# Performance work log

Hardware: AMD Instinct MI355X
Metric: run time of the kernel (lower is better)

The kernel has to match this reference:

```python
import jax, jax.numpy as jnp
import numpy as np

VOCAB = 4096   # vocab_size; must equal dim for weight + A@B to typecheck (as in source)
DIM = 4096
RANK = 256     # lora_rank
BATCH, SEQ = 4, 2048


def setup_inputs() -> dict:
    key = jax.random.key(0)
    k1, k2, k3, k4, k5 = jax.random.split(key, 5)
    x = jax.random.randint(k1, (BATCH, SEQ), 0, VOCAB)
    padding_mask = jax.random.randint(k2, (BATCH, SEQ), 0, 2).astype(bool)
    weight = jax.random.normal(k3, (VOCAB, DIM), dtype=jnp.float32) * 0.02
    A = jax.random.normal(k4, (VOCAB, RANK), dtype=jnp.float32) * 0.01
    B = jax.random.normal(k5, (RANK, VOCAB), dtype=jnp.float32) * 0.01
    return {"x": x, "padding_mask": padding_mask, "weight": weight, "A": A, "B": B}


def reference(x, padding_mask, weight, A, B):
    # world_size == 1, rank == 0 in the source module, so the distributed
    # index-shift / mask / all_reduce branches are no-ops.
    # lora_rank > 0 branch: embedding against the LoRA-corrected weight.
    # NOTE: faithful to source, A@B is [V, V] and requires DIM == VOCAB.
    corrected = weight + A @ B            # [V, DIM]
    y = corrected[x]                      # gather rows -> [B, S, DIM]
    # y[padding_mask] = 0
    y = jnp.where(padding_mask[..., None], jnp.zeros((), dtype=y.dtype), y)
    return y
```

## Files before the change

### kernel.cpp

```cpp
#include <hip/hip_runtime.h>
#include <stdint.h>

#define NTOK 8192
#define NCOL 4096
#define RANK 256
#define TPB  256
#define CPB  256

typedef __attribute__((ext_vector_type(8))) short bf16x8;
typedef __attribute__((ext_vector_type(4))) float f32x4;

__device__ __forceinline__ unsigned short f2bf(float f) {
    unsigned int u = __float_as_uint(f);
    u += 0x7fffu + ((u >> 16) & 1u);
    return (unsigned short)(u >> 16);
}

__global__ __launch_bounds__(256) void prep_kernel(
    const float* __restrict__ A, const float* __restrict__ B,
    unsigned short* __restrict__ Abf, unsigned short* __restrict__ Bfrag)
{
    if (blockIdx.x < 1024) {
        int i = blockIdx.x * 256 + threadIdx.x;
        float4 v = reinterpret_cast<const float4*>(A)[i];
        ushort4 o;
        o.x = f2bf(v.x); o.y = f2bf(v.y); o.z = f2bf(v.z); o.w = f2bf(v.w);
        reinterpret_cast<ushort4*>(Abf)[i] = o;
    } else {
        int gt = (blockIdx.x - 1024) * 256 + threadIdx.x;
        int ct = gt >> 9;
        int rem = gt & 511;
        int ks = rem >> 6;
        int ln = rem & 63;
        int col = ct * 16 + (ln & 15);
        int kb  = ks * 32 + ((ln >> 4) << 3);
        unsigned short pk[8];
        #pragma unroll
        for (int j = 0; j < 8; ++j)
            pk[j] = f2bf(B[(size_t)(kb + j) * NCOL + col]);
        uint4 o;
        o.x = (unsigned)pk[0] | ((unsigned)pk[1] << 16);
        o.y = (unsigned)pk[2] | ((unsigned)pk[3] << 16);
        o.z = (unsigned)pk[4] | ((unsigned)pk[5] << 16);
        o.w = (unsigned)pk[6] | ((unsigned)pk[7] << 16);
        reinterpret_cast<uint4*>(Bfrag)[gt] = o;
    }
}

__global__ __launch_bounds__(256) void emb_lora_mfma(
    const int* __restrict__ x,
    const int* __restrict__ mask,
    const float* __restrict__ W,
    const unsigned short* __restrict__ Abf,
    const unsigned short* __restrict__ Bfrag,
    float* __restrict__ out)
{
    __shared__ int s_idx[TPB];
    __shared__ int s_msk[TPB];

    const int tid  = threadIdx.x;
    const int lane = tid & 63;
    const int wave = tid >> 6;
    const int tok0 = blockIdx.x * TPB;
    const int col0 = blockIdx.y * CPB;

    s_idx[tid] = x[tok0 + tid];
    s_msk[tid] = mask[tok0 + tid];
    __syncthreads();

    bf16x8 af[4][8];
    #pragma unroll
    for (int g = 0; g < 4; ++g) {
        const int ar = s_idx[wave * 64 + g * 16 + (lane & 15)];
        const unsigned short* ap = Abf + (size_t)ar * RANK + ((lane >> 4) << 3);
        #pragma unroll
        for (int s = 0; s < 8; ++s)
            af[g][s] = *reinterpret_cast<const bf16x8*>(ap + s * 32);
    }

    const int colb = col0 + (lane & 15);
    unsigned mbits = 0;
    unsigned woff[4][4];
    unsigned obase[4];
    #pragma unroll
    for (int g = 0; g < 4; ++g) {
        const int rb = wave * 64 + g * 16 + ((lane >> 4) << 2);
        obase[g] = (unsigned)(tok0 + rb) * NCOL + colb;
        #pragma unroll
        for (int r = 0; r < 4; ++r) {
            mbits |= (s_msk[rb + r] ? 1u : 0u) << (g * 4 + r);
            woff[g][r] = (unsigned)s_idx[rb + r] * NCOL + colb;
        }
    }

    const uint4* bcol = reinterpret_cast<const uint4*>(Bfrag)
                        + (size_t)(blockIdx.y * 16) * 512 + lane;

    float wv[3][4][4];
    #pragma unroll
    for (int p = 0; p < 2; ++p) {
        #pragma unroll
        for (int g = 0; g < 4; ++g) {
            #pragma unroll
            for (int r = 0; r < 4; ++r) {
                float v = 0.0f;
                if (!((mbits >> (g * 4 + r)) & 1u)) v = W[woff[g][r] + p * 16];
                wv[p][g][r] = v;
            }
        }
    }

#define TILE_BODY(T, PF)                                                  \
    {                                                                     \
        const int t_ = (T);                                               \
        uint4 bb[4];                                                      \
        _Pragma("unroll")                                                 \
        for (int s = 0; s < 4; ++s)                                       \
            bb[s] = bcol[t_ * 512 + s * 64];                              \
        if (PF) {                                                         \
            _Pragma("unroll")                                             \
            for (int g = 0; g < 4; ++g) {                                 \
                _Pragma("unroll")                                         \
                for (int r = 0; r < 4; ++r) {                             \
                    float v = 0.0f;                                       \
                    if (!((mbits >> (g * 4 + r)) & 1u))                   \
                        v = W[woff[g][r] + (t_ + 2) * 16];                \
                    wv[(T + 2) % 3][g][r] = v;                            \
                }                                                         \
            }                                                             \
        }                                                                 \
        f32x4 acc[4];                                                     \
        _Pragma("unroll")                                                 \
        for (int g = 0; g < 4; ++g) acc[g] = (f32x4){0.f, 0.f, 0.f, 0.f}; \
        _Pragma("unroll")                                                 \
        for (int s = 0; s < 4; ++s) {                                     \
            bf16x8 b = __builtin_bit_cast(bf16x8, bb[s]);                 \
            _Pragma("unroll")                                             \
            for (int g = 0; g < 4; ++g)                                   \
                acc[g] = __builtin_amdgcn_mfma_f32_16x16x32_bf16(         \
                    af[g][s], b, acc[g], 0, 0, 0);                        \
        }                                                                 \
        _Pragma("unroll")                                                 \
        for (int s = 0; s < 4; ++s)                                       \
            bb[s] = bcol[t_ * 512 + (s + 4) * 64];                        \
        _Pragma("unroll")                                                 \
        for (int s = 0; s < 4; ++s) {                                     \
            bf16x8 b = __builtin_bit_cast(bf16x8, bb[s]);                 \
            _Pragma("unroll")                                             \
            for (int g = 0; g < 4; ++g)                                   \
                acc[g] = __builtin_amdgcn_mfma_f32_16x16x32_bf16(         \
                    af[g][s + 4], b, acc[g], 0, 0, 0);                    \
        }                                                                 \
        _Pragma("unroll")                                                 \
        for (int g = 0; g < 4; ++g) {                                     \
            _Pragma("unroll")                                             \
            for (int r = 0; r < 4; ++r) {                                 \
                float v = 0.0f;                                           \
                if (!((mbits >> (g * 4 + r)) & 1u))                       \
                    v = acc[g][r] + wv[(T) % 3][g][r];                    \
                out[obase[g] + r * NCOL + t_ * 16] = v;                   \
            }                                                             \
        }                                                                 \
    }

    TILE_BODY(0, 1);  TILE_BODY(1, 1);  TILE_BODY(2, 1);  TILE_BODY(3, 1);
    TILE_BODY(4, 1);  TILE_BODY(5, 1);  TILE_BODY(6, 1);  TILE_BODY(7, 1);
    TILE_BODY(8, 1);  TILE_BODY(9, 1);  TILE_BODY(10, 1); TILE_BODY(11, 1);
    TILE_BODY(12, 1); TILE_BODY(13, 1);
    TILE_BODY(14, 0); TILE_BODY(15, 0);
#undef TILE_BODY
}

extern "C" void kernel_launch(void* const* d_in, const int* in_sizes, int n_in,
                              void* d_out, int out_size, void* d_ws, size_t ws_size,
                              hipStream_t stream) {
    (void)in_sizes; (void)n_in; (void)out_size; (void)ws_size;

    const int*   x    = (const int*)d_in[0];
    const int*   mask = (const int*)d_in[1];
    const float* W    = (const float*)d_in[2];
    const float* A    = (const float*)d_in[3];
    const float* B    = (const float*)d_in[4];
    float*       out  = (float*)d_out;

    unsigned short* Abf   = (unsigned short*)d_ws;
    unsigned short* Bfrag = (unsigned short*)((char*)d_ws + (2u << 20));

    prep_kernel<<<dim3(1536), dim3(256), 0, stream>>>(A, B, Abf, Bfrag);

    dim3 grid(NTOK / TPB, NCOL / CPB);
    emb_lora_mfma<<<grid, dim3(256), 0, stream>>>(x, mask, W, Abf, Bfrag, out);
}
```

Before: 60.35 us.

## Transpose MFMA operands for float4 row-contiguous W loads and output stores

Swaps the A and B operands of the MFMA so each lane's accumulator holds four consecutive columns of one token row. W loads and output stores can then be 16-byte float4 accesses with one mask bit per row group instead of scalar strided ones. Columns per block are halved to 128, doubling the grid and re-gathering the A fragments twice as often, and the W prefetch ring shrinks from three stages to two.

New measurement: 72.62 us. 20.3% more time.

```diff
diff --git a/kernel.cpp b/kernel.cpp
--- a/kernel.cpp
+++ b/kernel.cpp
@@ -5,7 +5,7 @@
 #define NCOL 4096
 #define RANK 256
 #define TPB  256
-#define CPB  256
+#define CPB  128
 
 typedef __attribute__((ext_vector_type(8))) short bf16x8;
 typedef __attribute__((ext_vector_type(4))) float f32x4;
@@ -69,64 +69,59 @@
     __syncthreads();
 
     bf16x8 af[4][8];
+    int tokidx[4];
+    unsigned mb = 0;
     #pragma unroll
     for (int g = 0; g < 4; ++g) {
-        const int ar = s_idx[wave * 64 + g * 16 + (lane & 15)];
-        const unsigned short* ap = Abf + (size_t)ar * RANK + ((lane >> 4) << 3);
+        const int trow = wave * 64 + g * 16 + (lane & 15);
+        tokidx[g] = s_idx[trow];
+        mb |= (s_msk[trow] ? 1u : 0u) << g;
+        const unsigned short* ap = Abf + (size_t)tokidx[g] * RANK + ((lane >> 4) << 3);
         #pragma unroll
         for (int s = 0; s < 8; ++s)
             af[g][s] = *reinterpret_cast<const bf16x8*>(ap + s * 32);
     }
 
-    const int colb = col0 + (lane & 15);
-    unsigned mbits = 0;
-    unsigned woff[4][4];
-    unsigned obase[4];
+    const int colq = col0 + ((lane >> 4) << 2);
+    unsigned wq[4], oq[4];
     #pragma unroll
     for (int g = 0; g < 4; ++g) {
-        const int rb = wave * 64 + g * 16 + ((lane >> 4) << 2);
-        obase[g] = (unsigned)(tok0 + rb) * NCOL + colb;
-        #pragma unroll
-        for (int r = 0; r < 4; ++r) {
-            mbits |= (s_msk[rb + r] ? 1u : 0u) << (g * 4 + r);
-            woff[g][r] = (unsigned)s_idx[rb + r] * NCOL + colb;
-        }
+        const int trow = wave * 64 + g * 16 + (lane & 15);
+        wq[g] = ((unsigned)tokidx[g] * NCOL + colq) >> 2;
+        oq[g] = ((unsigned)(tok0 + trow) * NCOL + colq) >> 2;
     }
+    const float4* W4   = reinterpret_cast<const float4*>(W);
+    float4*       out4 = reinterpret_cast<float4*>(out);
 
     const uint4* bcol = reinterpret_cast<const uint4*>(Bfrag)
-                        + (size_t)(blockIdx.y * 16) * 512 + lane;
+                        + (size_t)(blockIdx.y * 8) * 512 + lane;
 
-    float wv[3][4][4];
+    float4 wv[2][4];
     #pragma unroll
     for (int p = 0; p < 2; ++p) {
         #pragma unroll
         for (int g = 0; g < 4; ++g) {
-            #pragma unroll
-            for (int r = 0; r < 4; ++r) {
-                float v = 0.0f;
-                if (!((mbits >> (g * 4 + r)) & 1u)) v = W[woff[g][r] + p * 16];
-                wv[p][g][r] = v;
-            }
+            float4 v = {0.f, 0.f, 0.f, 0.f};
+            if (!((mb >> g) & 1u)) v = W4[wq[g] + p * 4];
+            wv[p][g] = v;
         }
     }
 
 #define TILE_BODY(T, PF)                                                  \
     {                                                                     \
-        const int t_ = (T);                                               \
         uint4 bb[4];                                                      \
         _Pragma("unroll")                                                 \
         for (int s = 0; s < 4; ++s)                                       \
-            bb[s] = bcol[t_ * 512 + s * 64];                              \
+            bb[s] = bcol[(T) * 512 + s * 64];                             \
+        float4 wc[4];                                                     \
+        _Pragma("unroll")                                                 \
+        for (int g = 0; g < 4; ++g) wc[g] = wv[(T) & 1][g];               \
         if (PF) {                                                         \
             _Pragma("unroll")                                             \
             for (int g = 0; g < 4; ++g) {                                 \
-                _Pragma("unroll")                                         \
-                for (int r = 0; r < 4; ++r) {                             \
-                    float v = 0.0f;                                       \
-                    if (!((mbits >> (g * 4 + r)) & 1u))                   \
-                        v = W[woff[g][r] + (t_ + 2) * 16];                \
-                    wv[(T + 2) % 3][g][r] = v;                            \
-                }                                                         \
+                float4 v = {0.f, 0.f, 0.f, 0.f};                          \
+                if (!((mb >> g) & 1u)) v = W4[wq[g] + ((T) + 2) * 4];     \
+                wv[(T) & 1][g] = v;                                       \
             }                                                             \
         }                                                                 \
         f32x4 acc[4];                                                     \
@@ -138,36 +133,35 @@
             _Pragma("unroll")                                             \
             for (int g = 0; g < 4; ++g)                                   \
                 acc[g] = __builtin_amdgcn_mfma_f32_16x16x32_bf16(         \
-                    af[g][s], b, acc[g], 0, 0, 0);                        \
+                    b, af[g][s], acc[g], 0, 0, 0);                        \
         }                                                                 \
         _Pragma("unroll")                                                 \
         for (int s = 0; s < 4; ++s)                                       \
-            bb[s] = bcol[t_ * 512 + (s + 4) * 64];                        \
+            bb[s] = bcol[(T) * 512 + (s + 4) * 64];                       \
         _Pragma("unroll")                                                 \
         for (int s = 0; s < 4; ++s) {                                     \
             bf16x8 b = __builtin_bit_cast(bf16x8, bb[s]);                 \
             _Pragma("unroll")                                             \
             for (int g = 0; g < 4; ++g)                                   \
                 acc[g] = __builtin_amdgcn_mfma_f32_16x16x32_bf16(         \
-                    af[g][s + 4], b, acc[g], 0, 0, 0);                    \
+                    b, af[g][s + 4], acc[g], 0, 0, 0);                    \
         }                                                                 \
         _Pragma("unroll")                                                 \
         for (int g = 0; g < 4; ++g) {                                     \
-            _Pragma("unroll")                                             \
-            for (int r = 0; r < 4; ++r) {                                 \
-                float v = 0.0f;                                           \
-                if (!((mbits >> (g * 4 + r)) & 1u))                       \
-                    v = acc[g][r] + wv[(T) % 3][g][r];                    \
-                out[obase[g] + r * NCOL + t_ * 16] = v;                   \
+            float4 o = {0.f, 0.f, 0.f, 0.f};                              \
+            if (!((mb >> g) & 1u)) {                                      \
+                o.x = acc[g][0] + wc[g].x;                                \
+                o.y = acc[g][1] + wc[g].y;                                \
+                o.z = acc[g][2] + wc[g].z;                                \
+                o.w = acc[g][3] + wc[g].w;                                \
             }                                                             \
+            out4[oq[g] + (T) * 4] = o;                                    \
         }                                                                 \
     }
 
-    TILE_BODY(0, 1);  TILE_BODY(1, 1);  TILE_BODY(2, 1);  TILE_BODY(3, 1);
-    TILE_BODY(4, 1);  TILE_BODY(5, 1);  TILE_BODY(6, 1);  TILE_BODY(7, 1);
-    TILE_BODY(8, 1);  TILE_BODY(9, 1);  TILE_BODY(10, 1); TILE_BODY(11, 1);
-    TILE_BODY(12, 1); TILE_BODY(13, 1);
-    TILE_BODY(14, 0); TILE_BODY(15, 0);
+    TILE_BODY(0, 1); TILE_BODY(1, 1); TILE_BODY(2, 1);
+    TILE_BODY(3, 1); TILE_BODY(4, 1); TILE_BODY(5, 1);
+    TILE_BODY(6, 0); TILE_BODY(7, 0);
 #undef TILE_BODY
 }
 
```
